# Performance work log

Hardware: AMD Instinct MI355X
Metric: run time of the kernel (lower is better)

The kernel has to match this reference:

```python
import jax, jax.numpy as jnp
import numpy as np

SCALE = 100.0
ALPHA_MEM = 0.9
ALPHA_MEM_OUT = 0.9
ALPHA_R = 0.85
ALPHA_X = 0.95
ALPHA_P = 0.95
ALPHA_D = 0.95
WMIN = 0.0
WMAX = 2.0


@jax.custom_vjp
def spike_fn(x):
    # SurrGradSpike.forward: heaviside(x)
    return (x > 0).astype(x.dtype)

def _spike_fwd(x):
    return spike_fn(x), x

def _spike_bwd(x, g):
    # SurrGradSpike.backward: g / (scale*|x| + 1)^2
    return (g / (SCALE * jnp.abs(x) + 1.0) ** 2,)

spike_fn.defvjp(_spike_fwd, _spike_bwd)


def setup_inputs() -> dict:
    key = jax.random.key(0)
    ks = jax.random.split(key, 8)
    B, T, NI, N, NO, D = 8, 64, 256, 512, 32, 4
    inputs = jax.random.normal(ks[0], (B, T, NI), jnp.float32)
    w = jax.random.normal(ks[1], (N, N), jnp.float32) * (0.1 / np.sqrt(N))
    w_in = jax.random.normal(ks[2], (NI, N), jnp.float32) * (1.0 / np.sqrt(NI))
    w_out = jax.random.normal(ks[3], (N, NO), jnp.float32) * (1.0 / np.sqrt(N))
    # each synapse (e,o) assigned exactly one delay bin -> one-hot delay map (D,N,N)
    delay_idx = jax.random.randint(ks[4], (N, N), 0, D)
    dmap = jax.nn.one_hot(delay_idx, D, axis=0, dtype=jnp.float32)
    delays = jnp.array([1, 2, 3, 5], jnp.int32)
    w_signs = jnp.where(jnp.arange(N) < (4 * N) // 5, 1.0, -1.0).astype(jnp.float32)
    p = jax.random.uniform(ks[5], (N,), jnp.float32, minval=-0.5, maxval=0.5)
    A_p = jax.random.uniform(ks[6], (N, N), jnp.float32, minval=0.0, maxval=1e-3)
    A_d = jax.random.uniform(ks[7], (N, N), jnp.float32, minval=0.0, maxval=1e-3)
    return dict(inputs=inputs, w=w, w_in=w_in, w_out=w_out, dmap=dmap,
                delays=delays, w_signs=w_signs, p=p, A_p=A_p, A_d=A_d)


def _snn_forward(inputs, w, w_in, w_out, dmap, delays, w_signs, p, A_p, A_d):
    B, T, _ = inputs.shape
    N = w.shape[0]
    dt = inputs.dtype
    # epoch state
    inp = jnp.einsum('btc,cn->btn', inputs, w_in)          # (B,T,N)
    W = dmap * (w_signs[:, None] * jnp.abs(w))             # (D,N,N)
    p_depr = (p < 0).astype(dt)

    mem = jnp.zeros((B, N), dt)
    w_p = jnp.zeros((B, N), dt)
    x_bar = jnp.zeros((B, N), dt)
    u_pot = jnp.zeros((B, N), dt)
    u_dep = jnp.zeros((B, N), dt)
    w_stdp = jnp.ones((B, N, N), dt)
    rec_out = jnp.zeros((T, B, N), dt)
    rec_wp = jnp.zeros((T, B, N), dt)
    rec_xb = jnp.zeros((T, B, N), dt)

    def step(carry, xt):
        mem, w_p, x_bar, u_pot, u_dep, w_stdp, rec_out, rec_wp, rec_xb = carry
        t, inp_t = xt
        # mark_spikes + record_state (records pre-update values)
        spike = spike_fn(mem - 1.0)
        rec_out = rec_out.at[t].set(spike)
        rec_wp = rec_wp.at[t].set(w_p)
        rec_xb = rec_xb.at[t].set(x_bar)
        # delayed gathers; negative torch indices hit zero-initialized tail -> %T
        idx = (t - delays) % T
        out_del = jnp.take(rec_out, idx, axis=0)           # (D,B,N)
        wp_del = jnp.take(rec_wp, idx, axis=0)
        xb_del = jnp.take(rec_xb, idx, axis=0)
        # synaptic input
        syn_p = out_del * (1.0 + wp_del)
        syn = jnp.einsum('dbe,deo,beo->bo', syn_p, W, w_stdp)
        # STP
        dw_p = spike * p * (1.0 + p_depr * w_p)
        w_p = w_p * ALPHA_R + dw_p
        # STDP (uses pre-update u_dep/u_pot/mem)
        X = jnp.einsum('dbe,deo->beo', out_del, dmap)
        dW_dep = X * A_d[None] * jax.nn.relu(u_dep)[:, None, :]
        xbar_d = jnp.einsum('dbe,deo->beo', xb_del, dmap)
        dW_pot = xbar_d * A_p[None] * (jax.lax.stop_gradient(spike) * jax.nn.relu(u_pot))[:, None, :]
        x_bar = ALPHA_X * x_bar + (1.0 - ALPHA_X) * jax.lax.stop_gradient(spike)
        u_pot = ALPHA_P * u_pot + (1.0 - ALPHA_P) * mem
        u_dep = ALPHA_D * u_dep + (1.0 - ALPHA_D) * mem
        w_stdp = jnp.clip(w_stdp + dW_pot - dW_dep, WMIN, WMAX)
        # membrane integration with spike reset (detached)
        mem = ALPHA_MEM * mem + inp_t + syn - jax.lax.stop_gradient(spike)
        return (mem, w_p, x_bar, u_pot, u_dep, w_stdp, rec_out, rec_wp, rec_xb), None

    carry = (mem, w_p, x_bar, u_pot, u_dep, w_stdp, rec_out, rec_wp, rec_xb)
    xs = (jnp.arange(T), jnp.swapaxes(inp, 0, 1))
    carry, _ = jax.lax.scan(jax.checkpoint(step), carry, xs)
    rec_out = carry[6]                                     # (T,B,N)
    # readout: leaky integrator over projected spikes
    h2 = jnp.einsum('btn,no->bto', jnp.swapaxes(rec_out, 0, 1), w_out)

    def ro_step(o, h):
        o = ALPHA_MEM_OUT * o + h
        return o, o

    _, readout = jax.lax.scan(ro_step, jnp.zeros((B, h2.shape[-1]), dt),
                              jnp.swapaxes(h2, 0, 1))
    return jnp.swapaxes(readout, 0, 1)                     # (B,T,n_outputs)


def reference(inputs, w, w_in, w_out, dmap, delays, w_signs, p, A_p, A_d):
    return _snn_forward(inputs, w, w_in, w_out, dmap, delays, w_signs, p, A_p, A_d)
```

## Files before the change

kernel.cpp:

```cpp
#include <hip/hip_runtime.h>
#include <stdint.h>


#define B  8
#define T  64
#define NI 256
#define NN 512
#define NO 32
#define DD 4

#define NBLK 256
#define TPB  256
#define OPB  16
#define SPL  32
#define EPAD 516

#define REC_ELEMS (T*B*NN)

__device__ __forceinline__ unsigned long long rec_load(const unsigned long long* p) {
    return __hip_atomic_load(p, __ATOMIC_RELAXED, __HIP_MEMORY_SCOPE_AGENT);
}
__device__ __forceinline__ void rec_store(unsigned long long* p, unsigned long long v) {
    __hip_atomic_store(p, v, __ATOMIC_RELAXED, __HIP_MEMORY_SCOPE_AGENT);
}
__device__ __forceinline__ bool is_sentinel(unsigned long long v) {
    return (unsigned int)(v >> 32) == 0xFFFFFFFFu;
}

__global__ __launch_bounds__(TPB, 1)
void snn_main(const float* __restrict__ inputs,
              const float* __restrict__ w,
              const float* __restrict__ w_in,
              const float* __restrict__ dmap,
              const int*   __restrict__ delays,
              const float* __restrict__ w_signs,
              const float* __restrict__ p,
              const float* __restrict__ A_p,
              const float* __restrict__ A_d,
              unsigned long long* __restrict__ rec)
{
    __shared__ float2 sxq[DD*EPAD];
    __shared__ float  inp_s[T*OPB];
    __shared__ float  red[64];

    const int tid     = threadIdx.x;
    const int bid     = blockIdx.x;
    const int b       = bid & 7;
    const int chunk   = bid >> 3;
    const int o_base  = chunk * OPB;
    const int o_local = tid & 15;
    const int e_grp   = tid >> 4;
    const int o       = o_base + o_local;

    if (tid < OPB) {
        rec_store(rec + (size_t)(0*B + b)*NN + o_base + tid, 0ull);
    }

    float wv[SPL], ap[SPL], ad[SPL], ws[SPL];
    int   laddr[SPL];
    #pragma unroll
    for (int i = 0; i < SPL; ++i) {
        const int e = e_grp + 16*i;
        wv[i] = w_signs[e] * fabsf(w[e*NN + o]);
        ap[i] = A_p[e*NN + o];
        ad[i] = A_d[e*NN + o];
        int d = 0;
        if (dmap[1*NN*NN + e*NN + o] != 0.0f) d = 1;
        if (dmap[2*NN*NN + e*NN + o] != 0.0f) d = 2;
        if (dmap[3*NN*NN + e*NN + o] != 0.0f) d = 3;
        ws[i]    = 1.0f;
        laddr[i] = (d*EPAD + e) * 8;
    }
    int del[DD];
    #pragma unroll
    for (int d = 0; d < DD; ++d) del[d] = delays[d];

    {
        float* win = (float*)sxq;
        for (int k = tid; k < NI*OPB; k += TPB) {
            const int c = k >> 4, oo = k & 15;
            win[c*OPB + oo] = w_in[c*NN + o_base + oo];
        }
        __syncthreads();
        #pragma unroll
        for (int j = 0; j < 4; ++j) {
            const int tj = e_grp*4 + j;
            const float* inrow = inputs + (size_t)(b*T + tj)*NI;
            float a = 0.f;
            for (int c = 0; c < NI; ++c) a += inrow[c] * win[c*OPB + o_local];
            inp_s[tj*OPB + o_local] = a;
        }
        __syncthreads();
    }

    #pragma unroll
    for (int d = 0; d < DD; ++d) {
        sxq[d*EPAD + tid]       = make_float2(0.f, 0.f);
        sxq[d*EPAD + 256 + tid] = make_float2(0.f, 0.f);
    }
    __syncthreads();

    float mem = 0.f, w_p = 0.f, x_bar = 0.f, u_pot = 0.f, u_dep = 0.f;
    const float p_o  = p[o];
    const float pd_o = (p_o < 0.f) ? 1.f : 0.f;

    unsigned long long pf[DD][2];

    for (int t = 0; t < T; ++t) {
        if (t + 1 < T) {
            #pragma unroll
            for (int d = 0; d < DD; ++d) {
                if (del[d] > 1 && t + 1 >= del[d]) {
                    const int s = (t + 1 - del[d]) & 63;
                    const unsigned long long* src = rec + (size_t)(s*B + b)*NN + tid;
                    pf[d][0] = rec_load(src);
                    pf[d][1] = rec_load(src + 256);
                }
            }
        }

        const float spike = (mem > 1.0f) ? 1.0f : 0.0f;
        const float pg  = spike * fmaxf(u_pot, 0.f);
        const float udr = fmaxf(u_dep, 0.f);
        float acc = 0.f;
        #pragma unroll
        for (int i = 0; i < SPL; ++i) {
            const float2 v = *(const float2*)((const char*)sxq + laddr[i]);
            acc = fmaf(v.x, wv[i]*ws[i], acc);
            const unsigned int xu = __float_as_uint(v.y);
            const float dep = ((int)xu < 0) ? ad[i]*udr : 0.f;
            const float pot = (ap[i]*pg) * fabsf(v.y);
            ws[i] = fminf(fmaxf(ws[i] + pot - dep, 0.f), 2.f);
        }
        float a2 = acc + __shfl_xor(acc, 16);
        a2 += __shfl_xor(a2, 32);
        if ((tid & 63) < 16) red[(tid >> 6)*16 + o_local] = a2;
        __syncthreads();
        const float syn = red[o_local] + red[16 + o_local] + red[32 + o_local] + red[48 + o_local];

        const float wp_new = 0.85f*w_p + spike * p_o * (1.f + pd_o*w_p);
        const float xb_new = 0.95f*x_bar + 0.05f*spike;
        u_pot = 0.95f*u_pot + 0.05f*mem;
        u_dep = 0.95f*u_dep + 0.05f*mem;
        mem   = 0.9f*mem + inp_s[t*OPB + o_local] + syn - spike;
        w_p   = wp_new;
        x_bar = xb_new;

        if (t + 1 < T && tid < OPB) {
            const float spike1 = (mem > 1.0f) ? 1.0f : 0.0f;
            const float sp = spike1 * (1.f + w_p);
            const unsigned int xu = __float_as_uint(x_bar) | (spike1 != 0.f ? 0x80000000u : 0u);
            const unsigned long long pk =
                ((unsigned long long)xu << 32) | (unsigned int)__float_as_uint(sp);
            rec_store(rec + (size_t)((t+1)*B + b)*NN + o_base + tid, pk);
        }

        if (t + 1 < T) {
            #pragma unroll
            for (int d = 0; d < DD; ++d) {
                unsigned long long v0 = 0ull, v1 = 0ull;
                if (t + 1 >= del[d]) {
                    const int s = (t + 1 - del[d]) & 63;
                    const unsigned long long* src = rec + (size_t)(s*B + b)*NN + tid;
                    if (del[d] > 1) { v0 = pf[d][0]; v1 = pf[d][1]; }
                    else            { v0 = rec_load(src); v1 = rec_load(src + 256); }
                    int guard = 0;
                    while (is_sentinel(v0)) {
                        __builtin_amdgcn_s_sleep(1);
                        v0 = rec_load(src);
                        if (++guard > (1 << 24)) break;
                    }
                    guard = 0;
                    while (is_sentinel(v1)) {
                        __builtin_amdgcn_s_sleep(1);
                        v1 = rec_load(src + 256);
                        if (++guard > (1 << 24)) break;
                    }
                }
                sxq[d*EPAD + tid] =
                    make_float2(__uint_as_float((unsigned int)v0),
                                __uint_as_float((unsigned int)(v0 >> 32)));
                sxq[d*EPAD + 256 + tid] =
                    make_float2(__uint_as_float((unsigned int)v1),
                                make_float2(0.f,0.f).x + __uint_as_float((unsigned int)(v1 >> 32)));
            }
        }
        __syncthreads();
    }
}

__global__ __launch_bounds__(256)
void snn_h2(const unsigned long long* __restrict__ rec,
            const float* __restrict__ w_out,
            float* __restrict__ h2)
{
    const int bt = blockIdx.x;
    const int b = bt >> 6, t = bt & 63;
    const int tid = threadIdx.x;
    const int o = tid & 31, g = tid >> 5;
    const unsigned long long* ro = rec + (size_t)(t*B + b)*NN + g*64;
    float a = 0.f;
    #pragma unroll 8
    for (int j = 0; j < 64; ++j)
        if ((long long)ro[j] < 0) a += w_out[(g*64 + j)*NO + o];
    __shared__ float r2[8][NO];
    r2[g][o] = a;
    __syncthreads();
    if (tid < NO) {
        float s = 0.f;
        #pragma unroll
        for (int gg = 0; gg < 8; ++gg) s += r2[gg][tid];
        h2[bt*NO + tid] = s;
    }
}

__global__ void snn_scan(const float* __restrict__ h2, float* __restrict__ out)
{
    const int tid = threadIdx.x;
    const int b = tid >> 5, o = tid & 31;
    float st = 0.f;
    for (int t = 0; t < T; ++t) {
        st = 0.9f*st + h2[(b*T + t)*NO + o];
        out[(b*T + t)*NO + o] = st;
    }
}

extern "C" void kernel_launch(void* const* d_in, const int* in_sizes, int n_in,
                              void* d_out, int out_size, void* d_ws, size_t ws_size,
                              hipStream_t stream)
{
    const float* inputs  = (const float*)d_in[0];
    const float* w       = (const float*)d_in[1];
    const float* w_in    = (const float*)d_in[2];
    const float* w_out   = (const float*)d_in[3];
    const float* dmap    = (const float*)d_in[4];
    const int*   delays  = (const int*)  d_in[5];
    const float* w_signs = (const float*)d_in[6];
    const float* p       = (const float*)d_in[7];
    const float* A_p     = (const float*)d_in[8];
    const float* A_d     = (const float*)d_in[9];

    char* wsb = (char*)d_ws;
    unsigned long long* rec = (unsigned long long*)wsb;
    float* h2 = (float*)(wsb + (size_t)REC_ELEMS*8);

    hipMemsetAsync(rec, 0xFF, (size_t)REC_ELEMS*8, stream);

    hipLaunchKernelGGL(snn_main, dim3(NBLK), dim3(TPB), 0, stream,
                       inputs, w, w_in, dmap, delays, w_signs, p, A_p, A_d, rec);
    hipLaunchKernelGGL(snn_h2, dim3(B*T), dim3(256), 0, stream,
                       rec, w_out, h2);
    hipLaunchKernelGGL(snn_scan, dim3(1), dim3(256), 0, stream,
                       h2, (float*)d_out);
}
```

Before: 276.1 us.

## Fuse readout into main kernel, double-buffer spike planes, use wave-local reduction

Threads are remapped so each wave owns four output neurons, and the synaptic partial sums are reduced with wave shuffles instead of a shared-memory buffer plus a barrier. The shared spike-history plane is double-buffered, leaving one `__syncthreads` per timestep, and the delay-1 history is now prefetched like the other delays. The w_out projection and the leaky readout are folded into the main kernel: each block adds its per-chunk partial readout into the zeroed output with `atomicAdd`, which replaces the two follow-up kernels. The trade-off is extra float atomics, an extra memset of the output, and summation order that is no longer deterministic.

After: 305.2 us. 1.11x slower.

```diff
diff --git a/kernel.cpp b/kernel.cpp
--- a/kernel.cpp
+++ b/kernel.cpp
@@ -14,6 +14,7 @@
 #define OPB  16
 #define SPL  32
 #define EPAD 516
+#define PLANE (DD*EPAD)
 
 #define REC_ELEMS (T*B*NN)
 
@@ -25,6 +26,10 @@
 }
 __device__ __forceinline__ bool is_sentinel(unsigned long long v) {
     return (unsigned int)(v >> 32) == 0xFFFFFFFFu;
+}
+__device__ __forceinline__ float2 unpack_rec(unsigned long long v) {
+    return make_float2(__uint_as_float((unsigned int)v),
+                       __uint_as_float((unsigned int)(v >> 32)));
 }
 
 __global__ __launch_bounds__(TPB, 1)
@@ -37,24 +42,27 @@
               const float* __restrict__ p,
               const float* __restrict__ A_p,
               const float* __restrict__ A_d,
-              unsigned long long* __restrict__ rec)
+              const float* __restrict__ w_out,
+              unsigned long long* __restrict__ rec,
+              float* __restrict__ out)
 {
-    __shared__ float2 sxq[DD*EPAD];
+    __shared__ float2 sxq[2*PLANE];
     __shared__ float  inp_s[T*OPB];
-    __shared__ float  red[64];
+    __shared__ float  spike_s[2][OPB];
 
     const int tid     = threadIdx.x;
     const int bid     = blockIdx.x;
     const int b       = bid & 7;
     const int chunk   = bid >> 3;
     const int o_base  = chunk * OPB;
-    const int o_local = tid & 15;
-    const int e_grp   = tid >> 4;
+    const int lane    = tid & 63;
+    const int wave    = tid >> 6;
+    const int e_grp   = lane >> 2;
+    const int o_local = wave*4 + (lane & 3);
     const int o       = o_base + o_local;
-
-    if (tid < OPB) {
-        rec_store(rec + (size_t)(0*B + b)*NN + o_base + tid, 0ull);
-    }
+    const bool pub    = (e_grp == 0);
+
+    if (tid < OPB) rec_store(rec + (size_t)(0*B + b)*NN + o_base + tid, 0ull);
 
     float wv[SPL], ap[SPL], ad[SPL], ws[SPL];
     int   laddr[SPL];
@@ -75,6 +83,12 @@
     #pragma unroll
     for (int d = 0; d < DD; ++d) del[d] = delays[d];
 
+    float wo[OPB]; float ro_st = 0.f;
+    if (tid < NO) {
+        #pragma unroll
+        for (int j = 0; j < OPB; ++j) wo[j] = w_out[(o_base + j)*NO + tid];
+    }
+
     {
         float* win = (float*)sxq;
         for (int k = tid; k < NI*OPB; k += TPB) {
@@ -82,13 +96,14 @@
             win[c*OPB + oo] = w_in[c*NN + o_base + oo];
         }
         __syncthreads();
+        const int prow = tid >> 4, pcol = tid & 15;
         #pragma unroll
         for (int j = 0; j < 4; ++j) {
-            const int tj = e_grp*4 + j;
+            const int tj = prow*4 + j;
             const float* inrow = inputs + (size_t)(b*T + tj)*NI;
             float a = 0.f;
-            for (int c = 0; c < NI; ++c) a += inrow[c] * win[c*OPB + o_local];
-            inp_s[tj*OPB + o_local] = a;
+            for (int c = 0; c < NI; ++c) a += inrow[c] * win[c*OPB + pcol];
+            inp_s[tj*OPB + pcol] = a;
         }
         __syncthreads();
     }
@@ -110,7 +125,7 @@
         if (t + 1 < T) {
             #pragma unroll
             for (int d = 0; d < DD; ++d) {
-                if (del[d] > 1 && t + 1 >= del[d]) {
+                if (t + 1 >= del[d]) {
                     const int s = (t + 1 - del[d]) & 63;
                     const unsigned long long* src = rec + (size_t)(s*B + b)*NN + tid;
                     pf[d][0] = rec_load(src);
@@ -120,23 +135,37 @@
         }
 
         const float spike = (mem > 1.0f) ? 1.0f : 0.0f;
+        if (pub) spike_s[t & 1][o_local] = spike;
         const float pg  = spike * fmaxf(u_pot, 0.f);
         const float udr = fmaxf(u_dep, 0.f);
+
+        if (t >= 1 && tid < NO) {
+            float h = 0.f;
+            #pragma unroll
+            for (int j = 0; j < OPB; ++j) h = fmaf(spike_s[(t-1) & 1][j], wo[j], h);
+            ro_st = 0.9f*ro_st + h;
+            atomicAdd(out + ((size_t)b*T + (t-1))*NO + tid, ro_st);
+        }
+
+        const char* cbuf = (const char*)sxq + (t & 1)*(PLANE*8);
         float acc = 0.f;
         #pragma unroll
         for (int i = 0; i < SPL; ++i) {
-            const float2 v = *(const float2*)((const char*)sxq + laddr[i]);
+            const float2 v = *(const float2*)(cbuf + laddr[i]);
             acc = fmaf(v.x, wv[i]*ws[i], acc);
             const unsigned int xu = __float_as_uint(v.y);
             const float dep = ((int)xu < 0) ? ad[i]*udr : 0.f;
             const float pot = (ap[i]*pg) * fabsf(v.y);
             ws[i] = fminf(fmaxf(ws[i] + pot - dep, 0.f), 2.f);
         }
-        float a2 = acc + __shfl_xor(acc, 16);
-        a2 += __shfl_xor(a2, 32);
-        if ((tid & 63) < 16) red[(tid >> 6)*16 + o_local] = a2;
-        __syncthreads();
-        const float syn = red[o_local] + red[16 + o_local] + red[32 + o_local] + red[48 + o_local];
+        float a2 = acc + __shfl_xor(acc, 4);
+        a2 += __shfl_xor(a2, 8);
+        const int src0 = lane & 15;
+        const float p0 = __shfl(a2, src0);
+        const float p1 = __shfl(a2, src0 + 16);
+        const float p2 = __shfl(a2, src0 + 32);
+        const float p3 = __shfl(a2, src0 + 48);
+        const float syn = ((p0 + p1) + p2) + p3;
 
         const float wp_new = 0.85f*w_p + spike * p_o * (1.f + pd_o*w_p);
         const float xb_new = 0.95f*x_bar + 0.05f*spike;
@@ -146,24 +175,23 @@
         w_p   = wp_new;
         x_bar = xb_new;
 
-        if (t + 1 < T && tid < OPB) {
+        if (t + 1 < T && pub) {
             const float spike1 = (mem > 1.0f) ? 1.0f : 0.0f;
             const float sp = spike1 * (1.f + w_p);
             const unsigned int xu = __float_as_uint(x_bar) | (spike1 != 0.f ? 0x80000000u : 0u);
-            const unsigned long long pk =
-                ((unsigned long long)xu << 32) | (unsigned int)__float_as_uint(sp);
-            rec_store(rec + (size_t)((t+1)*B + b)*NN + o_base + tid, pk);
+            rec_store(rec + (size_t)((t+1)*B + b)*NN + o,
+                      ((unsigned long long)xu << 32) | (unsigned int)__float_as_uint(sp));
         }
 
         if (t + 1 < T) {
+            float2* wbuf = sxq + ((t+1) & 1)*PLANE;
             #pragma unroll
             for (int d = 0; d < DD; ++d) {
                 unsigned long long v0 = 0ull, v1 = 0ull;
                 if (t + 1 >= del[d]) {
                     const int s = (t + 1 - del[d]) & 63;
                     const unsigned long long* src = rec + (size_t)(s*B + b)*NN + tid;
-                    if (del[d] > 1) { v0 = pf[d][0]; v1 = pf[d][1]; }
-                    else            { v0 = rec_load(src); v1 = rec_load(src + 256); }
+                    v0 = pf[d][0]; v1 = pf[d][1];
                     int guard = 0;
                     while (is_sentinel(v0)) {
                         __builtin_amdgcn_s_sleep(1);
@@ -177,51 +205,19 @@
                         if (++guard > (1 << 24)) break;
                     }
                 }
-                sxq[d*EPAD + tid] =
-                    make_float2(__uint_as_float((unsigned int)v0),
-                                __uint_as_float((unsigned int)(v0 >> 32)));
-                sxq[d*EPAD + 256 + tid] =
-                    make_float2(__uint_as_float((unsigned int)v1),
-                                make_float2(0.f,0.f).x + __uint_as_float((unsigned int)(v1 >> 32)));
+                wbuf[d*EPAD + tid]       = unpack_rec(v0);
+                wbuf[d*EPAD + 256 + tid] = unpack_rec(v1);
             }
         }
         __syncthreads();
     }
-}
-
-__global__ __launch_bounds__(256)
-void snn_h2(const unsigned long long* __restrict__ rec,
-            const float* __restrict__ w_out,
-            float* __restrict__ h2)
-{
-    const int bt = blockIdx.x;
-    const int b = bt >> 6, t = bt & 63;
-    const int tid = threadIdx.x;
-    const int o = tid & 31, g = tid >> 5;
-    const unsigned long long* ro = rec + (size_t)(t*B + b)*NN + g*64;
-    float a = 0.f;
-    #pragma unroll 8
-    for (int j = 0; j < 64; ++j)
-        if ((long long)ro[j] < 0) a += w_out[(g*64 + j)*NO + o];
-    __shared__ float r2[8][NO];
-    r2[g][o] = a;
-    __syncthreads();
+
     if (tid < NO) {
-        float s = 0.f;
-        #pragma unroll
-        for (int gg = 0; gg < 8; ++gg) s += r2[gg][tid];
-        h2[bt*NO + tid] = s;
-    }
-}
-
-__global__ void snn_scan(const float* __restrict__ h2, float* __restrict__ out)
-{
-    const int tid = threadIdx.x;
-    const int b = tid >> 5, o = tid & 31;
-    float st = 0.f;
-    for (int t = 0; t < T; ++t) {
-        st = 0.9f*st + h2[(b*T + t)*NO + o];
-        out[(b*T + t)*NO + o] = st;
+        float h = 0.f;
+        #pragma unroll
+        for (int j = 0; j < OPB; ++j) h = fmaf(spike_s[(T-1) & 1][j], wo[j], h);
+        ro_st = 0.9f*ro_st + h;
+        atomicAdd(out + ((size_t)b*T + (T-1))*NO + tid, ro_st);
     }
 }
 
@@ -240,16 +236,13 @@
     const float* A_p     = (const float*)d_in[8];
     const float* A_d     = (const float*)d_in[9];
 
-    char* wsb = (char*)d_ws;
-    unsigned long long* rec = (unsigned long long*)wsb;
-    float* h2 = (float*)(wsb + (size_t)REC_ELEMS*8);
+    unsigned long long* rec = (unsigned long long*)d_ws;
+    float* out = (float*)d_out;
 
     hipMemsetAsync(rec, 0xFF, (size_t)REC_ELEMS*8, stream);
+    hipMemsetAsync(out, 0, (size_t)B*T*NO*4, stream);
 
     hipLaunchKernelGGL(snn_main, dim3(NBLK), dim3(TPB), 0, stream,
-                       inputs, w, w_in, dmap, delays, w_signs, p, A_p, A_d, rec);
-    hipLaunchKernelGGL(snn_h2, dim3(B*T), dim3(256), 0, stream,
-                       rec, w_out, h2);
-    hipLaunchKernelGGL(snn_scan, dim3(1), dim3(256), 0, stream,
-                       h2, (float*)d_out);
-}
+                       inputs, w, w_in, dmap, delays, w_signs, p, A_p, A_d,
+                       w_out, rec, out);
+}
```
